# Performance work log

Hardware: AMD Instinct MI355X
Metric: run time of the kernel (lower is better)

The kernel has to match this reference:

```python
import jax, jax.numpy as jnp
import numpy as np

N = 1024            # samples per branch
C = 64              # num_classes == embedding dim
MARGIN = 15.0       # self.margin and args.margin
LAM = 0.5           # args.lam
PROTOTYPE_POSITION = 1.0  # args.prototype_position
EPS_JS = 1e-8

def _cdist(a, b):
    # torch.cdist(p=2) via the gram trick; clamp for sqrt stability
    d2 = jnp.sum(a * a, axis=1)[:, None] + jnp.sum(b * b, axis=1)[None, :] - 2.0 * (a @ b.T)
    return jnp.sqrt(jnp.maximum(d2, 1e-12))

def _js_matrix(A, B):
    # pairwise Jensen-Shannon divergence: A [NA,C], B [NB,C] -> [NA,NB]
    A = A + EPS_JS
    B = B + EPS_JS
    logM = jnp.log((A[:, None, :] + B[None, :, :]) * 0.5)   # [NA,NB,C]
    kl_am = jnp.sum(A[:, None, :] * (jnp.log(A)[:, None, :] - logM), axis=-1)
    kl_bm = jnp.sum(B[None, :, :] * (jnp.log(B)[None, :, :] - logM), axis=-1)
    return 0.5 * kl_am + 0.5 * kl_bm

def _positive_branch(x, l_soft, x_prob):
    onehot = jnp.eye(C, dtype=x.dtype)
    # JS coefficient is computed via numpy in torch -> constant (no grad)
    js = jax.lax.stop_gradient(1.0 - _js_matrix(x_prob, onehot))       # [N, C]
    diff = x[:, None, :] - onehot * PROTOTYPE_POSITION                 # [N, C, C]
    pos_dist = jnp.sqrt(jnp.maximum(jnp.sum(diff * diff, axis=2), 1e-12))
    return jnp.sum(pos_dist * l_soft * js, axis=1)                     # [N]

def _ood_branch(x, branch_centers):
    d = _cdist(x, branch_centers)                                      # [N, C]
    ood_dist = jnp.maximum(MARGIN - d, 0.0)  # one_hot_labels are all ones
    coffi = jax.lax.stop_gradient(jnp.min(1.0 - ood_dist / MARGIN, axis=1))
    variance = jnp.sum((ood_dist / MARGIN) ** 2, axis=1)
    return variance * coffi                                            # [N]

def setup_inputs():
    key = jax.random.key(0)
    ks = jax.random.split(key, 6)
    x1 = jax.random.normal(ks[0], (N, C), jnp.float32)
    x2 = jax.random.normal(ks[1], (N, C), jnp.float32)
    x_prob1 = jax.nn.softmax(jax.random.normal(ks[2], (N, C), jnp.float32), axis=-1)
    x_prob2 = jax.nn.softmax(jax.random.normal(ks[3], (N, C), jnp.float32), axis=-1)
    l1 = jax.random.uniform(ks[4], (N, C), jnp.float32)
    l1 = l1 / jnp.sum(l1, axis=1, keepdims=True)
    l2 = jax.random.uniform(ks[5], (N, C), jnp.float32)
    l2 = l2 / jnp.sum(l2, axis=1, keepdims=True)
    # args.prototypes: class prototypes at scaled one-hot positions
    branch_centers = jnp.eye(C, dtype=jnp.float32) * PROTOTYPE_POSITION
    return {"x1": x1, "x2": x2, "x_prob1": x_prob1, "x_prob2": x_prob2,
            "l1": l1, "l2": l2, "branch_centers": branch_centers}

def reference(x1, x2, x_prob1, x_prob2, l1, l2, branch_centers):
    # positive loss
    posi = 0.5 * (jnp.sum(_positive_branch(x1, l1, x_prob1))
                  + jnp.sum(_positive_branch(x2, l2, x_prob2)))
    # negative loss
    neg_coffi = 1.0 - l1 @ l2.T                                        # [N, N]
    js = jax.lax.stop_gradient(_js_matrix(x_prob1, x_prob2))           # [N, N]
    ed = _cdist(x1, x2) + 1e-10
    pairs = jnp.maximum(MARGIN - ed, 0.0) * neg_coffi * js
    counts = jnp.sum(pairs > 0, axis=1)
    counts = jnp.where(counts == 0, 1, counts).astype(pairs.dtype)
    nega = jnp.sum(jnp.sum(pairs, axis=1) / counts)
    # ood loss
    ood = 0.5 * (jnp.sum(_ood_branch(x1, branch_centers))
                 + jnp.sum(_ood_branch(x2, branch_centers)))
    loss = posi + nega + LAM * ood
    return (loss, posi, nega)
```

## Files before the change

kernel.cpp:

```cpp
#include <hip/hip_runtime.h>

#define NN 1024
#define CC 64
#define MARGINF 15.0f
#define EPSJ 1e-8f
#define LN2F 0.69314718056f

#define C1_OFF   0
#define C2_OFF   (NN)
#define Q1_OFF   (2 * NN)
#define Q2_OFF   (3 * NN)
#define PP_OFF   (4 * NN)
#define OP_OFF   (4 * NN + 512)
#define NS_OFF   (4 * NN + 1024)
#define NC_OFF   (4 * NN + 1024 + 16 * NN)

__global__ __launch_bounds__(256) void fused_row_kernel(
    const float* __restrict__ x1, const float* __restrict__ x2,
    const float* __restrict__ p1, const float* __restrict__ p2,
    const float* __restrict__ l1, const float* __restrict__ l2,
    float* __restrict__ ws)
{
    const float S_B_CONST = -1.1595029e-5f;
    const float RSB_CONST = 1.00000064f;
    __shared__ float sposi[4], sood[4];

    int wave = (blockIdx.x * 256 + threadIdx.x) >> 6;
    int lane = threadIdx.x & 63;
    int wib  = threadIdx.x >> 6;
    int i = wave & (NN - 1);
    bool second = wave >= NN;
    const float* x = second ? x2 : x1;
    const float* p = second ? p2 : p1;
    const float* l = second ? l2 : l1;

    float P  = p[i * CC + lane];
    float xv = x[i * CC + lane];
    float lv = l[i * CC + lane];
    float A     = P + EPSJ;
    float AlogA = A * __logf(A);
    float t     = A + EPSJ;
    float tlogt = t * __logf(t);
    float xs    = xv * xv;

    float sA = AlogA, rsA = A, V = tlogt, q = xs;
    #pragma unroll
    for (int m = 32; m >= 1; m >>= 1) {
        sA  += __shfl_xor(sA,  m, 64);
        rsA += __shfl_xor(rsA, m, 64);
        V   += __shfl_xor(V,   m, 64);
        q   += __shfl_xor(q,   m, 64);
    }

    if (lane == 0) {
        ws[C1_OFF + (second ? NN : 0) + i] = sA + LN2F * rsA;
        ws[Q1_OFF + (second ? NN : 0) + i] = q;
    }

    float w = A + (1.0f + EPSJ);
    float sumslogs = V - tlogt + w * __logf(w);
    float js_div = 0.5f * (sA + S_B_CONST - sumslogs + LN2F * (rsA + RSB_CONST));
    float js = 1.0f - js_div;
    float pd = sqrtf(fmaxf(q - 2.0f * xv + 1.0f, 1e-12f));
    float posv = pd * lv * js;

    float od  = fmaxf(MARGINF - pd, 0.0f);
    float r   = od * (1.0f / MARGINF);
    float var = r * r;
    float cof = 1.0f - r;
    #pragma unroll
    for (int m = 32; m >= 1; m >>= 1) {
        posv += __shfl_xor(posv, m, 64);
        var  += __shfl_xor(var,  m, 64);
        cof   = fminf(cof, __shfl_xor(cof, m, 64));
    }
    if (lane == 0) {
        sposi[wib] = posv;
        sood[wib]  = var * cof;
    }
    __syncthreads();
    if (threadIdx.x == 0) {
        ws[PP_OFF + blockIdx.x] = sposi[0] + sposi[1] + sposi[2] + sposi[3];
        ws[OP_OFF + blockIdx.x] = sood[0] + sood[1] + sood[2] + sood[3];
    }
}

__global__ __launch_bounds__(256) void neg_kernel(
    const float* __restrict__ x1, const float* __restrict__ x2,
    const float* __restrict__ p1, const float* __restrict__ p2,
    const float* __restrict__ l1, const float* __restrict__ l2,
    float* __restrict__ ws)
{
    __shared__ float sx1[64][36], sp1[64][36], sl1[64][36];
    __shared__ float sx2[64][36], sp2[64][36], sl2[64][36];

    int t  = threadIdx.x;
    int bx = blockIdx.x, by = blockIdx.y;
    int i0 = by * 64, j0 = bx * 64;
    int tx = t & 15, ty = t >> 4;

    float K2[4][4];
    float G[4][4];
    float H[4][4];
    #pragma unroll
    for (int r = 0; r < 4; r++)
        #pragma unroll
        for (int s = 0; s < 4; s++) { K2[r][s] = 0.f; G[r][s] = 0.f; H[r][s] = 0.f; }

    for (int ph = 0; ph < 2; ++ph) {
        if (ph) __syncthreads();
        #pragma unroll
        for (int k = 0; k < 2; k++) {
            int f   = t + k * 256;
            int row = f >> 3;
            int col = (f & 7) * 4;
            int ga  = (i0 + row) * CC + ph * 32 + col;
            int gb  = (j0 + row) * CC + ph * 32 + col;
            float4 v;
            v = *(const float4*)&x1[ga];                         *(float4*)&sx1[row][col] = v;
            v = *(const float4*)&p1[ga];
            v.x += EPSJ; v.y += EPSJ; v.z += EPSJ; v.w += EPSJ;  *(float4*)&sp1[row][col] = v;
            v = *(const float4*)&l1[ga];                         *(float4*)&sl1[row][col] = v;
            v = *(const float4*)&x2[gb];                         *(float4*)&sx2[row][col] = v;
            v = *(const float4*)&p2[gb];
            v.x += EPSJ; v.y += EPSJ; v.z += EPSJ; v.w += EPSJ;  *(float4*)&sp2[row][col] = v;
            v = *(const float4*)&l2[gb];                         *(float4*)&sl2[row][col] = v;
        }
        __syncthreads();

        for (int cg = 0; cg < 8; ++cg) {
            int c = cg * 4;
            float4 ap[4], ax[4], alv[4], bp[4], bx4[4], blv[4];
            #pragma unroll
            for (int r = 0; r < 4; r++) {
                int ir = ty + 16 * r;
                int jr = tx + 16 * r;
                ap[r]  = *(float4*)&sp1[ir][c];
                ax[r]  = *(float4*)&sx1[ir][c];
                alv[r] = *(float4*)&sl1[ir][c];
                bp[r]  = *(float4*)&sp2[jr][c];
                bx4[r] = *(float4*)&sx2[jr][c];
                blv[r] = *(float4*)&sl2[jr][c];
            }
            #pragma unroll
            for (int r = 0; r < 4; r++) {
                #pragma unroll
                for (int s = 0; s < 4; s++) {
                    float sv;
                    sv = ap[r].x + bp[s].x; K2[r][s] = fmaf(sv, __log2f(sv), K2[r][s]);
                    G[r][s] = fmaf(ax[r].x, bx4[s].x, G[r][s]);
                    H[r][s] = fmaf(alv[r].x, blv[s].x, H[r][s]);
                    sv = ap[r].y + bp[s].y; K2[r][s] = fmaf(sv, __log2f(sv), K2[r][s]);
                    G[r][s] = fmaf(ax[r].y, bx4[s].y, G[r][s]);
                    H[r][s] = fmaf(alv[r].y, blv[s].y, H[r][s]);
                    sv = ap[r].z + bp[s].z; K2[r][s] = fmaf(sv, __log2f(sv), K2[r][s]);
                    G[r][s] = fmaf(ax[r].z, bx4[s].z, G[r][s]);
                    H[r][s] = fmaf(alv[r].z, blv[s].z, H[r][s]);
                    sv = ap[r].w + bp[s].w; K2[r][s] = fmaf(sv, __log2f(sv), K2[r][s]);
                    G[r][s] = fmaf(ax[r].w, bx4[s].w, G[r][s]);
                    H[r][s] = fmaf(alv[r].w, blv[s].w, H[r][s]);
                }
            }
        }
    }

    const float* c1 = ws + C1_OFF;
    const float* c2 = ws + C2_OFF;
    const float* q1 = ws + Q1_OFF;
    const float* q2 = ws + Q2_OFF;
    float* negS = ws + NS_OFF;
    float* negC = ws + NC_OFF;

    #pragma unroll
    for (int r = 0; r < 4; r++) {
        int gi = i0 + ty + 16 * r;
        float q1v = q1[gi], c1v = c1[gi];
        float psum = 0.0f, pcnt = 0.0f;
        #pragma unroll
        for (int s = 0; s < 4; s++) {
            int gj = j0 + tx + 16 * s;
            float ed = sqrtf(fmaxf(q1v + q2[gj] - 2.0f * G[r][s], 1e-12f)) + 1e-10f;
            float js = 0.5f * (c1v + c2[gj] - LN2F * K2[r][s]);
            float pair = fmaxf(MARGINF - ed, 0.0f) * (1.0f - H[r][s]) * js;
            psum += pair;
            pcnt += (pair > 0.0f) ? 1.0f : 0.0f;
        }
        #pragma unroll
        for (int m = 1; m <= 8; m <<= 1) {
            psum += __shfl_xor(psum, m, 64);
            pcnt += __shfl_xor(pcnt, m, 64);
        }
        if (tx == 0) {
            negS[gi * 16 + bx] = psum;
            negC[gi * 16 + bx] = pcnt;
        }
    }
}

__global__ __launch_bounds__(1024) void final_kernel(
    const float* __restrict__ ws, float* __restrict__ out)
{
    __shared__ float redv[16], redp[16], redo[16];
    int t = threadIdx.x;
    const float* rs = ws + NS_OFF + t * 16;
    const float* rc = ws + NC_OFF + t * 16;
    float s = 0.0f, c = 0.0f;
    #pragma unroll
    for (int k = 0; k < 4; k++) {
        float4 a = *(const float4*)&rs[k * 4];
        float4 b = *(const float4*)&rc[k * 4];
        s += (a.x + a.y) + (a.z + a.w);
        c += (b.x + b.y) + (b.z + b.w);
    }
    float v = s / fmaxf(c, 1.0f);
    float pp = (t < 512) ? ws[PP_OFF + t] : 0.0f;
    float oo = (t < 512) ? ws[OP_OFF + t] : 0.0f;
    #pragma unroll
    for (int m = 32; m >= 1; m >>= 1) {
        v  += __shfl_xor(v,  m, 64);
        pp += __shfl_xor(pp, m, 64);
        oo += __shfl_xor(oo, m, 64);
    }
    if ((t & 63) == 0) { redv[t >> 6] = v; redp[t >> 6] = pp; redo[t >> 6] = oo; }
    __syncthreads();
    if (t < 16) {
        float rv = redv[t], rp = redp[t], ro = redo[t];
        #pragma unroll
        for (int m = 8; m >= 1; m >>= 1) {
            rv += __shfl_xor(rv, m, 16);
            rp += __shfl_xor(rp, m, 16);
            ro += __shfl_xor(ro, m, 16);
        }
        if (t == 0) {
            float nega = rv;
            float posi = 0.5f * rp;
            float ood  = 0.5f * ro;
            out[0] = posi + nega + 0.5f * ood;
            out[1] = posi;
            out[2] = nega;
        }
    }
}

extern "C" void kernel_launch(void* const* d_in, const int* in_sizes, int n_in,
                              void* d_out, int out_size, void* d_ws, size_t ws_size,
                              hipStream_t stream) {
    const float* x1 = (const float*)d_in[0];
    const float* x2 = (const float*)d_in[1];
    const float* p1 = (const float*)d_in[2];
    const float* p2 = (const float*)d_in[3];
    const float* l1 = (const float*)d_in[4];
    const float* l2 = (const float*)d_in[5];
    float* ws  = (float*)d_ws;
    float* out = (float*)d_out;

    hipLaunchKernelGGL(fused_row_kernel, dim3(512), dim3(256), 0, stream,
                       x1, x2, p1, p2, l1, l2, ws);
    hipLaunchKernelGGL(neg_kernel, dim3(16, 16), dim3(256), 0, stream,
                       x1, x2, p1, p2, l1, l2, ws);
    hipLaunchKernelGGL(final_kernel, dim3(1), dim3(1024), 0, stream, ws, out);
}
```

Baseline: 88.76 us.

## Fuse per-row prologue kernel into the pairwise negative kernel

Removes the separate row kernel and folds its work into the pairwise tile kernel. Each block recomputes the per-row JS constants and squared norms for its own 64+64 rows into shared memory, and also takes a slice of the positive and OOD row reductions. This drops one kernel launch and the global workspace round trip for the row constants. In exchange, the row statistics are recomputed 16 times redundantly, and each block runs a serial 32-iteration shuffle-reduction prologue before its main tile loop starts.

After: 105.1 us. 18.4% more time.

```diff
diff --git a/kernel.cpp b/kernel.cpp
--- a/kernel.cpp
+++ b/kernel.cpp
@@ -6,84 +6,10 @@
 #define EPSJ 1e-8f
 #define LN2F 0.69314718056f
 
-#define C1_OFF   0
-#define C2_OFF   (NN)
-#define Q1_OFF   (2 * NN)
-#define Q2_OFF   (3 * NN)
-#define PP_OFF   (4 * NN)
-#define OP_OFF   (4 * NN + 512)
-#define NS_OFF   (4 * NN + 1024)
-#define NC_OFF   (4 * NN + 1024 + 16 * NN)
-
-__global__ __launch_bounds__(256) void fused_row_kernel(
-    const float* __restrict__ x1, const float* __restrict__ x2,
-    const float* __restrict__ p1, const float* __restrict__ p2,
-    const float* __restrict__ l1, const float* __restrict__ l2,
-    float* __restrict__ ws)
-{
-    const float S_B_CONST = -1.1595029e-5f;
-    const float RSB_CONST = 1.00000064f;
-    __shared__ float sposi[4], sood[4];
-
-    int wave = (blockIdx.x * 256 + threadIdx.x) >> 6;
-    int lane = threadIdx.x & 63;
-    int wib  = threadIdx.x >> 6;
-    int i = wave & (NN - 1);
-    bool second = wave >= NN;
-    const float* x = second ? x2 : x1;
-    const float* p = second ? p2 : p1;
-    const float* l = second ? l2 : l1;
-
-    float P  = p[i * CC + lane];
-    float xv = x[i * CC + lane];
-    float lv = l[i * CC + lane];
-    float A     = P + EPSJ;
-    float AlogA = A * __logf(A);
-    float t     = A + EPSJ;
-    float tlogt = t * __logf(t);
-    float xs    = xv * xv;
-
-    float sA = AlogA, rsA = A, V = tlogt, q = xs;
-    #pragma unroll
-    for (int m = 32; m >= 1; m >>= 1) {
-        sA  += __shfl_xor(sA,  m, 64);
-        rsA += __shfl_xor(rsA, m, 64);
-        V   += __shfl_xor(V,   m, 64);
-        q   += __shfl_xor(q,   m, 64);
-    }
-
-    if (lane == 0) {
-        ws[C1_OFF + (second ? NN : 0) + i] = sA + LN2F * rsA;
-        ws[Q1_OFF + (second ? NN : 0) + i] = q;
-    }
-
-    float w = A + (1.0f + EPSJ);
-    float sumslogs = V - tlogt + w * __logf(w);
-    float js_div = 0.5f * (sA + S_B_CONST - sumslogs + LN2F * (rsA + RSB_CONST));
-    float js = 1.0f - js_div;
-    float pd = sqrtf(fmaxf(q - 2.0f * xv + 1.0f, 1e-12f));
-    float posv = pd * lv * js;
-
-    float od  = fmaxf(MARGINF - pd, 0.0f);
-    float r   = od * (1.0f / MARGINF);
-    float var = r * r;
-    float cof = 1.0f - r;
-    #pragma unroll
-    for (int m = 32; m >= 1; m >>= 1) {
-        posv += __shfl_xor(posv, m, 64);
-        var  += __shfl_xor(var,  m, 64);
-        cof   = fminf(cof, __shfl_xor(cof, m, 64));
-    }
-    if (lane == 0) {
-        sposi[wib] = posv;
-        sood[wib]  = var * cof;
-    }
-    __syncthreads();
-    if (threadIdx.x == 0) {
-        ws[PP_OFF + blockIdx.x] = sposi[0] + sposi[1] + sposi[2] + sposi[3];
-        ws[OP_OFF + blockIdx.x] = sood[0] + sood[1] + sood[2] + sood[3];
-    }
-}
+#define PP_OFF   0
+#define OP_OFF   256
+#define NS_OFF   512
+#define NC_OFF   (512 + 16 * NN)
 
 __global__ __launch_bounds__(256) void neg_kernel(
     const float* __restrict__ x1, const float* __restrict__ x2,
@@ -93,12 +19,92 @@
 {
     __shared__ float sx1[64][36], sp1[64][36], sl1[64][36];
     __shared__ float sx2[64][36], sp2[64][36], sl2[64][36];
+    __shared__ float sc1[64], sq1[64], sc2[64], sq2[64];
+    __shared__ float spos[4], sood[4];
+
+    const float S_B_CONST = -1.1595029e-5f;
+    const float RSB_CONST = 1.00000064f;
 
     int t  = threadIdx.x;
     int bx = blockIdx.x, by = blockIdx.y;
     int i0 = by * 64, j0 = bx * 64;
+    int w    = t >> 6;
+    int lane = t & 63;
+
+    {
+        const float* xa = (w < 2) ? x1 : x2;
+        const float* pa = (w < 2) ? p1 : p2;
+        int   base  = (w < 2) ? i0 : j0;
+        float* cdst = (w < 2) ? sc1 : sc2;
+        float* qdst = (w < 2) ? sq1 : sq2;
+        int loc0 = (w & 1) * 32;
+        for (int r = 0; r < 32; ++r) {
+            int loc = loc0 + r;
+            float P  = pa[(base + loc) * CC + lane];
+            float xv = xa[(base + loc) * CC + lane];
+            float a  = P + EPSJ;
+            float al = a * __logf(a);
+            float xs = xv * xv;
+            #pragma unroll
+            for (int m = 32; m >= 1; m >>= 1) {
+                al += __shfl_xor(al, m, 64);
+                a  += __shfl_xor(a,  m, 64);
+                xs += __shfl_xor(xs, m, 64);
+            }
+            if (lane == 0) { cdst[loc] = al + LN2F * a; qdst[loc] = xs; }
+        }
+    }
+
+    {
+        int b = by * 16 + bx;
+        float pacc = 0.0f, oacc = 0.0f;
+        #pragma unroll
+        for (int k = 0; k < 2; ++k) {
+            int job = 8 * b + 2 * w + k;
+            int i = job & (NN - 1);
+            bool second = job >= NN;
+            const float* x = second ? x2 : x1;
+            const float* p = second ? p2 : p1;
+            const float* l = second ? l2 : l1;
+            float P  = p[i * CC + lane];
+            float xv = x[i * CC + lane];
+            float lv = l[i * CC + lane];
+            float A     = P + EPSJ;
+            float AlogA = A * __logf(A);
+            float tt    = A + EPSJ;
+            float tlogt = tt * __logf(tt);
+            float xs    = xv * xv;
+            float sA = AlogA, rsA = A, V = tlogt, q = xs;
+            #pragma unroll
+            for (int m = 32; m >= 1; m >>= 1) {
+                sA  += __shfl_xor(sA,  m, 64);
+                rsA += __shfl_xor(rsA, m, 64);
+                V   += __shfl_xor(V,   m, 64);
+                q   += __shfl_xor(q,   m, 64);
+            }
+            float ww = A + (1.0f + EPSJ);
+            float sumslogs = V - tlogt + ww * __logf(ww);
+            float js_div = 0.5f * (sA + S_B_CONST - sumslogs + LN2F * (rsA + RSB_CONST));
+            float js = 1.0f - js_div;
+            float pd = sqrtf(fmaxf(q - 2.0f * xv + 1.0f, 1e-12f));
+            float posv = pd * lv * js;
+            float od  = fmaxf(MARGINF - pd, 0.0f);
+            float rr  = od * (1.0f / MARGINF);
+            float var = rr * rr;
+            float cof = 1.0f - rr;
+            #pragma unroll
+            for (int m = 32; m >= 1; m >>= 1) {
+                posv += __shfl_xor(posv, m, 64);
+                var  += __shfl_xor(var,  m, 64);
+                cof   = fminf(cof, __shfl_xor(cof, m, 64));
+            }
+            pacc += posv;
+            oacc += var * cof;
+        }
+        if (lane == 0) { spos[w] = pacc; sood[w] = oacc; }
+    }
+
     int tx = t & 15, ty = t >> 4;
-
     float K2[4][4];
     float G[4][4];
     float H[4][4];
@@ -127,6 +133,11 @@
             v = *(const float4*)&l2[gb];                         *(float4*)&sl2[row][col] = v;
         }
         __syncthreads();
+
+        if (ph == 0 && t == 0) {
+            ws[PP_OFF + by * 16 + bx] = spos[0] + spos[1] + spos[2] + spos[3];
+            ws[OP_OFF + by * 16 + bx] = sood[0] + sood[1] + sood[2] + sood[3];
+        }
 
         for (int cg = 0; cg < 8; ++cg) {
             int c = cg * 4;
@@ -164,23 +175,20 @@
         }
     }
 
-    const float* c1 = ws + C1_OFF;
-    const float* c2 = ws + C2_OFF;
-    const float* q1 = ws + Q1_OFF;
-    const float* q2 = ws + Q2_OFF;
     float* negS = ws + NS_OFF;
     float* negC = ws + NC_OFF;
 
     #pragma unroll
     for (int r = 0; r < 4; r++) {
-        int gi = i0 + ty + 16 * r;
-        float q1v = q1[gi], c1v = c1[gi];
+        int li = ty + 16 * r;
+        int gi = i0 + li;
+        float q1v = sq1[li], c1v = sc1[li];
         float psum = 0.0f, pcnt = 0.0f;
         #pragma unroll
         for (int s = 0; s < 4; s++) {
-            int gj = j0 + tx + 16 * s;
-            float ed = sqrtf(fmaxf(q1v + q2[gj] - 2.0f * G[r][s], 1e-12f)) + 1e-10f;
-            float js = 0.5f * (c1v + c2[gj] - LN2F * K2[r][s]);
+            int lj = tx + 16 * s;
+            float ed = sqrtf(fmaxf(q1v + sq2[lj] - 2.0f * G[r][s], 1e-12f)) + 1e-10f;
+            float js = 0.5f * (c1v + sc2[lj] - LN2F * K2[r][s]);
             float pair = fmaxf(MARGINF - ed, 0.0f) * (1.0f - H[r][s]) * js;
             psum += pair;
             pcnt += (pair > 0.0f) ? 1.0f : 0.0f;
@@ -213,8 +221,8 @@
         c += (b.x + b.y) + (b.z + b.w);
     }
     float v = s / fmaxf(c, 1.0f);
-    float pp = (t < 512) ? ws[PP_OFF + t] : 0.0f;
-    float oo = (t < 512) ? ws[OP_OFF + t] : 0.0f;
+    float pp = (t < 256) ? ws[PP_OFF + t] : 0.0f;
+    float oo = (t < 256) ? ws[OP_OFF + t] : 0.0f;
     #pragma unroll
     for (int m = 32; m >= 1; m >>= 1) {
         v  += __shfl_xor(v,  m, 64);
@@ -254,8 +262,6 @@
     float* ws  = (float*)d_ws;
     float* out = (float*)d_out;
 
-    hipLaunchKernelGGL(fused_row_kernel, dim3(512), dim3(256), 0, stream,
-                       x1, x2, p1, p2, l1, l2, ws);
     hipLaunchKernelGGL(neg_kernel, dim3(16, 16), dim3(256), 0, stream,
                        x1, x2, p1, p2, l1, l2, ws);
     hipLaunchKernelGGL(final_kernel, dim3(1), dim3(1024), 0, stream, ws, out);
```
